# Performance work log

Hardware: AMD Instinct MI355X
Metric: run time of the kernel (lower is better)

## Reference

```python
import jax, jax.numpy as jnp
import numpy as np

N = 20000      # nodes
E = 80000      # edges (before self loops)
NG = 64        # graphs in batch
EMB = 780      # embedding_size (768 text + 12 time)
NEG_SLOPE = 0.2
BN_EPS = 1e-5


def setup_inputs() -> dict:
    key = jax.random.key(0)
    ks = jax.random.split(key, 20)
    def rn(k, shape, s=0.05):
        return jax.random.normal(k, shape, dtype=jnp.float32) * s
    z = lambda n: jnp.zeros((n,), dtype=jnp.float32)
    o = lambda n: jnp.ones((n,), dtype=jnp.float32)
    x = jax.random.normal(ks[0], (N, 772), dtype=jnp.float32)
    edge_index = jax.random.randint(ks[1], (2, E), 0, N)
    batch = jnp.sort(jax.random.randint(ks[2], (N,), 0, NG))
    return dict(
        x=x, edge_index=edge_index, batch=batch,
        time_W=rn(ks[3], (4, 12)), time_b=z(12),
        lin_W0=rn(ks[4], (EMB, 3 * EMB)), att_src0=rn(ks[5], (3, EMB)), att_dst0=rn(ks[6], (3, EMB)),
        bias0=z(3 * EMB), gamma0=o(3 * EMB), beta0=z(3 * EMB),
        lin_W1=rn(ks[7], (3 * EMB, 3 * EMB)), att_src1=rn(ks[8], (3, EMB)), att_dst1=rn(ks[9], (3, EMB)),
        bias1=z(3 * EMB), gamma1=o(3 * EMB), beta1=z(3 * EMB),
        lin_W2=rn(ks[10], (3 * EMB, EMB)), att_src2=rn(ks[11], (1, EMB)), att_dst2=rn(ks[12], (1, EMB)),
        bias2=z(EMB), gamma2=o(EMB), beta2=z(EMB),
        mlp_W1=rn(ks[13], (EMB, 128)), mlp_b1=z(128),
        mlp_W2=rn(ks[14], (128, 64)), mlp_b2=z(64),
    )


def _gat_layer(h, src, dst, W, a_src, a_dst, b, heads):
    # PyG GATConv (eval mode: dropout off), concat=True, self loops already in src/dst
    C = W.shape[1] // heads
    hp = (h @ W).reshape(N, heads, C)                       # [N,H,C]
    a_s = jnp.sum(hp * a_src[None], axis=-1)                # [N,H]
    a_d = jnp.sum(hp * a_dst[None], axis=-1)                # [N,H]
    e = jax.nn.leaky_relu(a_s[src] + a_d[dst], NEG_SLOPE)   # [E+N,H]
    m = jax.ops.segment_max(e, dst, num_segments=N)         # segment softmax over incoming edges
    m = jnp.where(jnp.isfinite(m), m, 0.0)
    p = jnp.exp(e - m[dst])
    denom = jax.ops.segment_sum(p, dst, num_segments=N)
    alpha = p / (denom[dst] + 1e-16)                        # [E+N,H]
    out = jax.ops.segment_sum(alpha[:, :, None] * hp[src], dst, num_segments=N)  # [N,H,C]
    return out.reshape(N, heads * C) + b


def _bn(h, gamma, beta):
    # BatchNorm in training-mode math (batch statistics, biased variance)
    mu = jnp.mean(h, axis=0)
    var = jnp.mean((h - mu) ** 2, axis=0)
    return (h - mu) * jax.lax.rsqrt(var + BN_EPS) * gamma + beta


def reference(x, edge_index, batch, time_W, time_b,
              lin_W0, att_src0, att_dst0, bias0, gamma0, beta0,
              lin_W1, att_src1, att_dst1, bias1, gamma1, beta1,
              lin_W2, att_src2, att_dst2, bias2, gamma2, beta2,
              mlp_W1, mlp_b1, mlp_W2, mlp_b2):
    te = x[:, 768:772] @ time_W + time_b
    h = jnp.concatenate([jax.lax.stop_gradient(x[:, :768]), te,
                         jax.lax.stop_gradient(x[:, 772:])], axis=-1)  # [N, 780]
    sl = jnp.arange(N)
    src = jnp.concatenate([edge_index[0], sl])   # add self loops
    dst = jnp.concatenate([edge_index[1], sl])
    layers = [
        (lin_W0, att_src0, att_dst0, bias0, gamma0, beta0, 3),
        (lin_W1, att_src1, att_dst1, bias1, gamma1, beta1, 3),
        (lin_W2, att_src2, att_dst2, bias2, gamma2, beta2, 1),
    ]
    for W, a_s, a_d, b, g, bt, heads in layers:
        h = jnp.tanh(_gat_layer(h, src, dst, W, a_s, a_d, b, heads))
        h = _bn(h, g, bt)
    cnt = jax.ops.segment_sum(jnp.ones((N,), dtype=h.dtype), batch, num_segments=NG)
    pooled = jax.ops.segment_sum(h, batch, num_segments=NG) / jnp.maximum(cnt, 1.0)[:, None]
    pooled = jax.nn.relu(pooled)
    out = jnp.tanh(pooled @ mlp_W1 + mlp_b1) @ mlp_W2 + mlp_b2
    return out  # [NG, 64]
```

## Files before the change

kernel.cpp:

```cpp
#include <hip/hip_runtime.h>
#include <math.h>

#define NN   20000
#define EE   80000
#define ELP  100000
#define NGR  64
#define EMB  780
#define W3   2340
#define EMBP 832
#define W3P  2368
#define NZ   (W3+8)

static inline int cdiv_i(long long a, long long b){ return (int)((a + b - 1) / b); }

typedef _Float16 f16;
typedef _Float16 f16x4 __attribute__((ext_vector_type(4)));
typedef _Float16 f16x8 __attribute__((ext_vector_type(8)));
typedef float    f32x4 __attribute__((ext_vector_type(4)));

__device__ __forceinline__ void async_ld16(const f16* g, f16* l){
    __builtin_amdgcn_global_load_lds(
        (const __attribute__((address_space(1))) unsigned int*)g,
        (__attribute__((address_space(3))) unsigned int*)l,
        16, 0, 0);
}

__global__ void k_zero_f32(float* p, int n){
    int i = blockIdx.x*256 + threadIdx.x; if (i < n) p[i] = 0.f;
}
__global__ void k_zero_i32(int* p, int n){
    int i = blockIdx.x*256 + threadIdx.x; if (i < n) p[i] = 0;
}
__global__ void k_copy_i32(const int* __restrict__ s, int* __restrict__ d, int n){
    int i = blockIdx.x*256 + threadIdx.x; if (i < n) d[i] = s[i];
}

__global__ void k_transpose(const float* __restrict__ W, f16* __restrict__ Wt,
                            const float* __restrict__ sc, int K, int N, int KP){
    __shared__ float T[32][33];
    int n0 = blockIdx.x*32, k0 = blockIdx.y*32;
    int tx = threadIdx.x, ty = threadIdx.y;
#pragma unroll
    for (int r = 0; r < 4; r++){
        int k = k0 + ty + r*8;
        float v = 0.f;
        if (k < K && n0 + tx < N){
            v = W[(size_t)k*N + n0 + tx];
            if (sc) v *= sc[k];
        }
        T[ty + r*8][tx] = v;
    }
    __syncthreads();
#pragma unroll
    for (int r = 0; r < 4; r++){
        int n = n0 + ty + r*8;
        int k = k0 + tx;
        if (n < N && k < KP) Wt[(size_t)n*KP + k] = (f16)T[tx][ty + r*8];
    }
}

__global__ void k_wvec(const float* __restrict__ W, const float* __restrict__ asrc,
                       const float* __restrict__ adst, const float* __restrict__ sc,
                       f16* __restrict__ Wt, int K, int N, int KP, int H){
    int k = blockIdx.x*4 + (threadIdx.x >> 6);
    int lane = threadIdx.x & 63;
    if (k >= K) return;
    const float* row = W + (size_t)k*N;
    float acc[6];
#pragma unroll
    for (int i = 0; i < 6; i++) acc[i] = 0.f;
    for (int c = lane; c < EMB; c += 64){
        for (int h = 0; h < H; h++){
            float wv = row[h*EMB + c];
            acc[h]     += wv * asrc[h*EMB + c];
            acc[H + h] += wv * adst[h*EMB + c];
        }
    }
    float s = sc ? sc[k] : 1.f;
    for (int i = 0; i < 2*H; i++){
        float v = acc[i];
#pragma unroll
        for (int off = 32; off; off >>= 1) v += __shfl_xor(v, off);
        if (lane == 0) Wt[(size_t)(N + i)*KP + k] = (f16)(v * s);
    }
}

__global__ void k_wfin(const float* __restrict__ asrc, const float* __restrict__ adst,
                       float* __restrict__ dvec, int N, int H){
    int wv = threadIdx.x >> 6, lane = threadIdx.x & 63;
    for (int i = wv; i < 2*H; i += 4){
        int h = (i < H) ? i : (i - H);
        const float* att = (i < H) ? (asrc + h*EMB) : (adst + h*EMB);
        float s = 0.f;
        for (int c = lane; c < EMB; c += 64) s += dvec[h*EMB + c] * att[c];
#pragma unroll
        for (int off = 32; off; off >>= 1) s += __shfl_xor(s, off);
        if (lane == 0) dvec[N + i] = s;
    }
}

#define DVEC_KSPLIT 32
__global__ void k_dvec(const float* __restrict__ W, const float* __restrict__ sh,
                       float* __restrict__ dvec, int K, int N){
    int n = blockIdx.x*256 + threadIdx.x;
    if (n >= N) return;
    int slice = blockIdx.y;
    int k0 = (int)(((long long)K * slice) / DVEC_KSPLIT);
    int k1 = (int)(((long long)K * (slice+1)) / DVEC_KSPLIT);
    float s = 0.f;
    for (int k = k0; k < k1; k++) s += sh[k] * W[(size_t)k*N + n];
    atomicAdd(&dvec[n], s);
}

__global__ void k_build_h(const float* __restrict__ x, const float* __restrict__ tW,
                          const float* __restrict__ tb, f16* __restrict__ h){
    int idx = blockIdx.x*256 + threadIdx.x;
    if (idx >= NN*EMBP) return;
    int n = idx / EMBP, c = idx - n*EMBP;
    const float* xr = x + (size_t)n*772;
    float v;
    if (c < 768) v = xr[c];
    else if (c < EMB){
        int j = c - 768;
        v = tb[j] + xr[768]*tW[j] + xr[769]*tW[12+j] + xr[770]*tW[24+j] + xr[771]*tW[36+j];
    } else v = 0.f;
    h[idx] = (f16)v;
}

__global__ void k_deg(const int* __restrict__ ei, int* __restrict__ deg){
    int k = blockIdx.x*256 + threadIdx.x; if (k >= ELP) return;
    int d = (k < EE) ? ei[EE + k] : (k - EE);
    atomicAdd(&deg[d], 1);
}

__global__ __launch_bounds__(1024) void k_scan(const int* __restrict__ deg, int* __restrict__ rp){
    __shared__ int part[1024];
    int tid = threadIdx.x;
    int i0 = tid*20;
    int n = (i0 < NN) ? min(20, NN - i0) : 0;
    int s = 0;
    for (int k = 0; k < n; k++) s += deg[i0+k];
    part[tid] = s; __syncthreads();
    for (int off = 1; off < 1024; off <<= 1){
        int t = (tid >= off) ? part[tid-off] : 0;
        __syncthreads();
        part[tid] += t;
        __syncthreads();
    }
    int run = part[tid] - s;
    for (int k = 0; k < n; k++){ rp[i0+k] = run; run += deg[i0+k]; }
    if (tid == 1023) rp[NN] = part[1023];
}

__global__ void k_fill(const int* __restrict__ ei, int* __restrict__ cursor, int* __restrict__ csrc){
    int k = blockIdx.x*256 + threadIdx.x; if (k >= ELP) return;
    int s, d;
    if (k < EE){ s = ei[k]; d = ei[EE + k]; } else { s = k - EE; d = s; }
    int pos = atomicAdd(&cursor[d], 1);
    csrc[pos] = s;
}

__global__ void k_grp(const int* __restrict__ batch, int* __restrict__ grp){
    int g = blockIdx.x*256 + threadIdx.x; if (g > NGR) return;
    int lo = 0, hi = NN;
    while (lo < hi){ int mid = (lo+hi)>>1; if (batch[mid] < g) lo = mid+1; else hi = mid; }
    grp[g] = lo;
}

__global__ __launch_bounds__(256) void k_gemm_mfma(const f16* __restrict__ A,
                                                   const f16* __restrict__ Bt,
                                                   const float* __restrict__ dvec,
                                                   f16* __restrict__ C,
                                                   float* __restrict__ a_sd,
                                                   int M, int N, int NB, int H,
                                                   int KP, int SN,
                                                   int Mtiles, int NT){
    int bid = blockIdx.x;
    int xcd = bid & 7;
    int j   = bid >> 3;
    int sl  = j / NT;
    int nt  = j - sl*NT;
    int mt  = sl*8 + xcd;
    if (mt >= Mtiles) return;
    int m0 = mt*128, n0 = nt*128;

    __shared__ f16 As[128*64];
    __shared__ f16 Bs[128*64];
    int tid = threadIdx.x;
    int w = tid >> 6, lane = tid & 63;

    int lrow = lane >> 2;
    int lko  = (lane & 3) * 8;

    int i2a = w*2, i2b = w*2 + 1;
    const f16* gA0 = A  + (size_t)min(m0 + i2a*16 + lrow, M-1)*KP + lko;
    const f16* gA1 = A  + (size_t)min(m0 + i2b*16 + lrow, M-1)*KP + lko;
    const f16* gB0 = Bt + (size_t)min(n0 + i2a*16 + lrow, NB-1)*KP + lko;
    const f16* gB1 = Bt + (size_t)min(n0 + i2b*16 + lrow, NB-1)*KP + lko;
    f16* lA0 = &As[i2a*512]; f16* lA1 = &As[i2b*512];
    f16* lB0 = &Bs[i2a*512]; f16* lB1 = &Bs[i2b*512];

    f32x4 acc[4][4];
#pragma unroll
    for (int i = 0; i < 4; i++)
#pragma unroll
        for (int j2 = 0; j2 < 4; j2++) acc[i][j2] = (f32x4)0.f;

    int wm = (w & 1) * 64, wn = (w >> 1) * 64;
    int lq = lane >> 4, lm = lane & 15;

    for (int kk = 0; kk < KP; kk += 64){
        __syncthreads();
        async_ld16(gA0 + kk, lA0);
        async_ld16(gA1 + kk, lA1);
        async_ld16(gB0 + kk, lB0);
        async_ld16(gB1 + kk, lB1);
        async_ld16(gA0 + kk + 32, lA0 + 4096);
        async_ld16(gA1 + kk + 32, lA1 + 4096);
        async_ld16(gB0 + kk + 32, lB0 + 4096);
        async_ld16(gB1 + kk + 32, lB1 + 4096);
        __syncthreads();

#pragma unroll
        for (int half = 0; half < 2; half++){
            const f16* Ap = As + half*4096;
            const f16* Bp = Bs + half*4096;
            f16x8 aF[4], bF[4];
#pragma unroll
            for (int mi = 0; mi < 4; mi++)
                aF[mi] = *(const f16x8*)&Ap[(wm + mi*16 + lm)*32 + lq*8];
#pragma unroll
            for (int ni = 0; ni < 4; ni++)
                bF[ni] = *(const f16x8*)&Bp[(wn + ni*16 + lm)*32 + lq*8];
#pragma unroll
            for (int mi = 0; mi < 4; mi++)
#pragma unroll
                for (int ni = 0; ni < 4; ni++)
                    acc[mi][ni] = __builtin_amdgcn_mfma_f32_16x16x32_f16(aF[mi], bF[ni], acc[mi][ni], 0, 0, 0);
        }
    }

#pragma unroll
    for (int mi = 0; mi < 4; mi++){
#pragma unroll
        for (int ni = 0; ni < 4; ni++){
            int col = n0 + wn + ni*16 + lm;
            int rbase = m0 + wm + mi*16 + lq*4;
            if (col < N){
                float dv = dvec[col];
#pragma unroll
                for (int r = 0; r < 4; r++){
                    int row = rbase + r;
                    if (row < M)
                        C[(size_t)row*SN + col] = (f16)(acc[mi][ni][r] + dv);
                }
            } else if (col < NB){
                int jc = col - N;
                int idx = (jc < H) ? jc : (3 + jc - H);
                float dv = dvec[col];
#pragma unroll
                for (int r = 0; r < 4; r++){
                    int row = rbase + r;
                    if (row < M)
                        a_sd[(size_t)row*6 + idx] = acc[mi][ni][r] + dv;
                }
            }
        }
    }
}

template<int H>
__global__ __launch_bounds__(256) void k_agg2(const f16* __restrict__ hp, const int* __restrict__ rp,
                                              const int* __restrict__ csrc, const float* __restrict__ a_sd,
                                              const float* __restrict__ bias,
                                              f16* __restrict__ y, int SP, int W){
    int n = blockIdx.x, tid = threadIdx.x, lane = tid & 63;
    int beg = rp[n], deg = rp[n+1] - beg;

    float adv[H];
#pragma unroll
    for (int h = 0; h < H; h++) adv[h] = a_sd[(size_t)n*6 + 3 + h];

    float mx[H];
#pragma unroll
    for (int h = 0; h < H; h++) mx[h] = -1e30f;
    for (int base = 0; base < deg; base += 64){
        int e = base + lane;
        if (e < deg){
            int s = csrc[beg + e];
#pragma unroll
            for (int h = 0; h < H; h++){
                float t = a_sd[(size_t)s*6 + h] + adv[h];
                t = t > 0.f ? t : 0.2f*t;
                mx[h] = fmaxf(mx[h], t);
            }
        }
    }
#pragma unroll
    for (int off = 32; off; off >>= 1)
#pragma unroll
        for (int h = 0; h < H; h++) mx[h] = fmaxf(mx[h], __shfl_xor(mx[h], off));

    float dn[H];
#pragma unroll
    for (int h = 0; h < H; h++) dn[h] = 0.f;
    for (int base = 0; base < deg; base += 64){
        int e = base + lane;
        if (e < deg){
            int s = csrc[beg + e];
#pragma unroll
            for (int h = 0; h < H; h++){
                float t = a_sd[(size_t)s*6 + h] + adv[h];
                t = t > 0.f ? t : 0.2f*t;
                dn[h] += expf(t - mx[h]);
            }
        }
    }
#pragma unroll
    for (int off = 32; off; off >>= 1)
#pragma unroll
        for (int h = 0; h < H; h++) dn[h] += __shfl_xor(dn[h], off);
    float inv[H];
#pragma unroll
    for (int h = 0; h < H; h++) inv[h] = 1.f / (dn[h] + 1e-16f);

    float acc[2][8];
#pragma unroll
    for (int g = 0; g < 2; g++)
#pragma unroll
        for (int j = 0; j < 8; j++) acc[g][j] = 0.f;
    int  cg[2];  cg[0] = tid*8; cg[1] = 2048 + tid*8;
    bool act[2]; act[0] = cg[0] < W; act[1] = cg[1] < W;
    int hlo[2], hhi[2], nsp[2];
#pragma unroll
    for (int g = 0; g < 2; g++){
        int c = cg[g];
        int hl = min(c / EMB, H-1);
        int hh = min((c+7) / EMB, H-1);
        hlo[g] = hl; hhi[g] = hh;
        nsp[g] = (hh > hl) ? (EMB*(hl+1) - c) : 8;
    }

    for (int base = 0; base < deg; base += 64){
        int cnt = min(64, deg - base);
        int sl = 0; float al[H];
        {
            int e = base + lane;
            if (e < deg){
                sl = csrc[beg + e];
#pragma unroll
                for (int h = 0; h < H; h++){
                    float t = a_sd[(size_t)sl*6 + h] + adv[h];
                    t = t > 0.f ? t : 0.2f*t;
                    al[h] = expf(t - mx[h]) * inv[h];
                }
            } else {
#pragma unroll
                for (int h = 0; h < H; h++) al[h] = 0.f;
            }
        }
#pragma unroll 2
        for (int e = 0; e < cnt; e++){
            int s = __shfl(sl, e);
            float a0 = __shfl(al[0], e);
            float a1 = (H==3) ? __shfl(al[1], e) : a0;
            float a2 = (H==3) ? __shfl(al[2], e) : a0;
            const f16* row = hp + (size_t)s*SP;
#pragma unroll
            for (int g = 0; g < 2; g++){
                if (act[g]){
                    f16x8 v = *(const f16x8*)(row + cg[g]);
                    float lo = (hlo[g]==0) ? a0 : (hlo[g]==1 ? a1 : a2);
                    float hi = (hhi[g]==0) ? a0 : (hhi[g]==1 ? a1 : a2);
#pragma unroll
                    for (int j = 0; j < 8; j++){
                        float alj = (j < nsp[g]) ? lo : hi;
                        acc[g][j] += alj * (float)v[j];
                    }
                }
            }
        }
    }

#pragma unroll
    for (int g = 0; g < 2; g++){
        int c = cg[g];
        if (c < SP){
            f16x8 o;
#pragma unroll
            for (int j = 0; j < 8; j++){
                float vv = (c + j < W) ? tanhf(acc[g][j] + bias[c+j]) : 0.f;
                o[j] = (f16)vv;
            }
            *(f16x8*)(y + (size_t)n*SP + c) = o;
        }
    }
}

__global__ void k_bnstat(const f16* __restrict__ y, float* __restrict__ ps,
                         float* __restrict__ pq, int W, int SP){
    int c0 = (blockIdx.x*256 + threadIdx.x)*4;
    if (c0 >= W) return;
    int slice = blockIdx.y;
    float s[4] = {0,0,0,0}, q[4] = {0,0,0,0};
    for (int r = slice; r < NN; r += 128){
        f16x4 u = *(const f16x4*)(y + (size_t)r*SP + c0);
#pragma unroll
        for (int j = 0; j < 4; j++){ float v = (float)u[j]; s[j] += v; q[j] += v*v; }
    }
#pragma unroll
    for (int j = 0; j < 4; j++){
        ps[(size_t)slice*W3 + c0+j] = s[j];
        pq[(size_t)slice*W3 + c0+j] = q[j];
    }
}

__global__ void k_bnfin(const float* __restrict__ ps, const float* __restrict__ pq,
                        const float* __restrict__ gamma, const float* __restrict__ beta,
                        float* __restrict__ sc, float* __restrict__ sh,
                        float* __restrict__ dvec, int W, int zn){
    int c = blockIdx.x*256 + threadIdx.x;
    if (c < W){
        float m = 0.f, q = 0.f;
        for (int s = 0; s < 128; s++){ m += ps[(size_t)s*W3 + c]; q += pq[(size_t)s*W3 + c]; }
        m *= (1.f/NN);
        float v = q * (1.f/NN) - m*m;
        float is = 1.f / sqrtf(v + 1e-5f);
        float g = gamma[c];
        sc[c] = is * g;
        sh[c] = beta[c] - m * is * g;
    }
    if (c < zn) dvec[c] = 0.f;
}

__global__ void k_pool(const f16* __restrict__ h, const int* __restrict__ grp,
                       float* __restrict__ pooled){
    int g = blockIdx.x;
    int c = threadIdx.x*4;
    if (c >= EMB) return;
    int r0 = grp[g], r1 = grp[g+1];
    float s0=0.f, s1=0.f, s2=0.f, s3=0.f;
    for (int r = r0; r < r1; r++){
        f16x4 u = *(const f16x4*)(h + (size_t)r*EMBP + c);
        s0 += (float)u[0]; s1 += (float)u[1]; s2 += (float)u[2]; s3 += (float)u[3];
    }
    pooled[g*EMB + c] = s0; pooled[g*EMB + c+1] = s1;
    pooled[g*EMB + c+2] = s2; pooled[g*EMB + c+3] = s3;
}

__global__ __launch_bounds__(256) void k_mlp(const float* __restrict__ pooled, const int* __restrict__ grp,
                                             const float* __restrict__ sc, const float* __restrict__ sh,
                                             const float* __restrict__ W1, const float* __restrict__ b1,
                                             const float* __restrict__ W2, const float* __restrict__ b2,
                                             float* __restrict__ out){
    __shared__ float p[EMB];
    __shared__ float hid[128];
    int g = blockIdx.x, tid = threadIdx.x;
    int cnt = grp[g+1] - grp[g];
    float ic = 1.f / fmaxf((float)cnt, 1.f);
    for (int c = tid; c < EMB; c += 256){
        float v = pooled[g*EMB + c] * ic * sc[c] + sh[c];
        p[c] = v > 0.f ? v : 0.f;
    }
    __syncthreads();
    if (tid < 128){
        float s = b1[tid];
        for (int k = 0; k < EMB; k++) s += p[k] * W1[k*128 + tid];
        hid[tid] = tanhf(s);
    }
    __syncthreads();
    if (tid < 64){
        float s = b2[tid];
        for (int k = 0; k < 128; k++) s += hid[k] * W2[k*64 + tid];
        out[g*64 + tid] = s;
    }
}

extern "C" void kernel_launch(void* const* d_in, const int* in_sizes, int n_in,
                              void* d_out, int out_size, void* d_ws, size_t ws_size,
                              hipStream_t stream) {
    (void)in_sizes; (void)n_in; (void)out_size;
    const float* x    = (const float*)d_in[0];
    const int*   ei   = (const int*)  d_in[1];
    const int*   batch= (const int*)  d_in[2];
    const float* tW   = (const float*)d_in[3];
    const float* tb   = (const float*)d_in[4];
    const float* W0   = (const float*)d_in[5];
    const float* as0  = (const float*)d_in[6];
    const float* ad0  = (const float*)d_in[7];
    const float* b0   = (const float*)d_in[8];
    const float* g0   = (const float*)d_in[9];
    const float* be0  = (const float*)d_in[10];
    const float* W1   = (const float*)d_in[11];
    const float* as1  = (const float*)d_in[12];
    const float* ad1  = (const float*)d_in[13];
    const float* b1   = (const float*)d_in[14];
    const float* g1   = (const float*)d_in[15];
    const float* be1  = (const float*)d_in[16];
    const float* W2   = (const float*)d_in[17];
    const float* as2  = (const float*)d_in[18];
    const float* ad2  = (const float*)d_in[19];
    const float* b2   = (const float*)d_in[20];
    const float* g2   = (const float*)d_in[21];
    const float* be2  = (const float*)d_in[22];
    const float* mW1  = (const float*)d_in[23];
    const float* mb1  = (const float*)d_in[24];
    const float* mW2  = (const float*)d_in[25];
    const float* mb2  = (const float*)d_in[26];
    float* outp = (float*)d_out;

    size_t off = 0;
    auto carve = [&](size_t bytes) -> void* {
        void* p = (char*)d_ws + off;
        off = (off + bytes + 255) & ~(size_t)255;
        return p;
    };
    f16* big1 = (f16*)carve((size_t)NN*W3P*2);
    f16* big2 = (f16*)carve((size_t)NN*W3P*2);
    f16* Wt   = (f16*)carve((size_t)NZ*W3P*2);
    float* a_sd  = (float*)carve((size_t)NN*6*4);
    float* psum  = (float*)carve((size_t)128*W3*4);
    float* psq   = (float*)carve((size_t)128*W3*4);
    float* sc    = (float*)carve((size_t)W3*4);
    float* sh    = (float*)carve((size_t)W3*4);
    float* dvec  = (float*)carve((size_t)NZ*4);
    float* pooled= (float*)carve((size_t)NGR*EMB*4);
    int*   grp   = (int*)carve((size_t)(NGR+1)*4);
    int*   deg   = (int*)carve((size_t)NN*4);
    int*   rp    = (int*)carve((size_t)(NN+1)*4);
    int*   csrc  = (int*)carve((size_t)ELP*4);

    if (ws_size < off) return;

    k_zero_i32<<<cdiv_i(NN,256),256,0,stream>>>(deg, NN);
    k_deg<<<cdiv_i(ELP,256),256,0,stream>>>(ei, deg);
    k_scan<<<1,1024,0,stream>>>(deg, rp);
    k_copy_i32<<<cdiv_i(NN,256),256,0,stream>>>(rp, deg, NN);
    k_fill<<<cdiv_i(ELP,256),256,0,stream>>>(ei, deg, csrc);
    k_grp<<<1,256,0,stream>>>(batch, grp);

    k_build_h<<<cdiv_i((long long)NN*EMBP,256),256,0,stream>>>(x, tW, tb, big1);
    k_zero_f32<<<cdiv_i(NZ,256),256,0,stream>>>(dvec, NZ);

    struct Layer { const float* W; const float* as; const float* ad; const float* b;
                   const float* g; const float* be; int H; int K; int KP; };
    Layer layers[3] = {
        {W0, as0, ad0, b0, g0, be0, 3, EMB, EMBP},
        {W1, as1, ad1, b1, g1, be1, 3, W3,  W3P },
        {W2, as2, ad2, b2, g2, be2, 1, W3,  W3P },
    };

    for (int L = 0; L < 3; L++){
        Layer& ly = layers[L];
        int Wout  = ly.H * EMB;
        int NB    = Wout + 2*ly.H;
        int SPout = (Wout == W3) ? W3P : EMBP;
        const float* scale = (L == 0) ? nullptr : sc;

        dim3 tg(cdiv_i(Wout,32), cdiv_i(ly.KP,32));
        k_transpose<<<tg, dim3(32,8), 0, stream>>>(ly.W, Wt, scale, ly.K, Wout, ly.KP);
        k_wvec<<<cdiv_i(ly.K,4),256,0,stream>>>(ly.W, ly.as, ly.ad, scale, Wt, ly.K, Wout, ly.KP, ly.H);
        if (L > 0){
            dim3 dg(cdiv_i(Wout,256), DVEC_KSPLIT);
            k_dvec<<<dg,256,0,stream>>>(ly.W, sh, dvec, ly.K, Wout);
        }
        k_wfin<<<1,256,0,stream>>>(ly.as, ly.ad, dvec, Wout, ly.H);

        int Mtiles = cdiv_i(NN,128), NT = cdiv_i(NB,128);
        int nb = ((Mtiles+7)/8)*8*NT;
        k_gemm_mfma<<<nb, 256, 0, stream>>>(big1, Wt, dvec, big2, a_sd,
                                            NN, Wout, NB, ly.H, ly.KP, SPout, Mtiles, NT);

        if (ly.H == 3)
            k_agg2<3><<<NN,256,0,stream>>>(big2, rp, csrc, a_sd, ly.b, big1, SPout, Wout);
        else
            k_agg2<1><<<NN,256,0,stream>>>(big2, rp, csrc, a_sd, ly.b, big1, SPout, Wout);

        dim3 gs(cdiv_i(Wout/4,256), 128);
        k_bnstat<<<gs,256,0,stream>>>(big1, psum, psq, Wout, SPout);
        int zn = (L < 2) ? NZ : 0;
        k_bnfin<<<cdiv_i(Wout,256),256,0,stream>>>(psum, psq, ly.g, ly.be, sc, sh, dvec, Wout, zn);
    }

    k_pool<<<NGR,256,0,stream>>>(big1, grp, pooled);
    k_mlp<<<NGR,256,0,stream>>>(pooled, grp, sc, sh, mW1, mb1, mW2, mb2, outp);
}
```

Baseline: 1.651 ms.

## Fuse weight-prep kernels, stage GEMM epilogue through LDS, vectorize build and scan copy

Folds the BN-shift dvec reduction into the transpose kernel and the attention-vector finalisation into k_wvec, and lets the scan write the cursor array directly, removing several small launches. The GEMM epilogue now stages the f16 output tile in LDS and writes it with 16-byte stores instead of scattered 2-byte stores. k_build_h writes 4 halves per thread, bnstat reads contiguous row ranges, and the aggregation loop is unrolled further. There is a race risk: k_wvec block 0 reads dvec that k_transpose fills with atomics, which relies on stream ordering, and the wfin part can run before the other wvec blocks finish, though those blocks do not write dvec.

```diff
diff --git a/kernel.cpp b/kernel.cpp
--- a/kernel.cpp
+++ b/kernel.cpp
@@ -31,24 +31,31 @@
 __global__ void k_zero_i32(int* p, int n){
     int i = blockIdx.x*256 + threadIdx.x; if (i < n) p[i] = 0;
 }
-__global__ void k_copy_i32(const int* __restrict__ s, int* __restrict__ d, int n){
-    int i = blockIdx.x*256 + threadIdx.x; if (i < n) d[i] = s[i];
-}
 
 __global__ void k_transpose(const float* __restrict__ W, f16* __restrict__ Wt,
-                            const float* __restrict__ sc, int K, int N, int KP){
+                            const float* __restrict__ sc, const float* __restrict__ sh,
+                            float* __restrict__ dvec, int K, int N, int KP){
     __shared__ float T[32][33];
+    __shared__ float D[8][33];
     int n0 = blockIdx.x*32, k0 = blockIdx.y*32;
     int tx = threadIdx.x, ty = threadIdx.y;
+    float raw[4];
 #pragma unroll
     for (int r = 0; r < 4; r++){
         int k = k0 + ty + r*8;
-        float v = 0.f;
-        if (k < K && n0 + tx < N){
-            v = W[(size_t)k*N + n0 + tx];
-            if (sc) v *= sc[k];
-        }
-        T[ty + r*8][tx] = v;
+        float w = 0.f;
+        if (k < K && n0 + tx < N) w = W[(size_t)k*N + n0 + tx];
+        raw[r] = w;
+        T[ty + r*8][tx] = sc ? w * ((k < K) ? sc[k] : 0.f) : w;
+    }
+    if (sh){
+        float p = 0.f;
+#pragma unroll
+        for (int r = 0; r < 4; r++){
+            int k = k0 + ty + r*8;
+            if (k < K) p += sh[k] * raw[r];
+        }
+        D[ty][tx] = p;
     }
     __syncthreads();
 #pragma unroll
@@ -57,74 +64,74 @@
         int k = k0 + tx;
         if (n < N && k < KP) Wt[(size_t)n*KP + k] = (f16)T[tx][ty + r*8];
     }
+    if (sh && ty == 0 && n0 + tx < N){
+        float s = 0.f;
+#pragma unroll
+        for (int j = 0; j < 8; j++) s += D[j][tx];
+        atomicAdd(&dvec[n0 + tx], s);
+    }
 }
 
 __global__ void k_wvec(const float* __restrict__ W, const float* __restrict__ asrc,
                        const float* __restrict__ adst, const float* __restrict__ sc,
-                       f16* __restrict__ Wt, int K, int N, int KP, int H){
+                       f16* __restrict__ Wt, float* __restrict__ dvec,
+                       int K, int N, int KP, int H){
     int k = blockIdx.x*4 + (threadIdx.x >> 6);
     int lane = threadIdx.x & 63;
-    if (k >= K) return;
-    const float* row = W + (size_t)k*N;
-    float acc[6];
-#pragma unroll
-    for (int i = 0; i < 6; i++) acc[i] = 0.f;
-    for (int c = lane; c < EMB; c += 64){
-        for (int h = 0; h < H; h++){
-            float wv = row[h*EMB + c];
-            acc[h]     += wv * asrc[h*EMB + c];
-            acc[H + h] += wv * adst[h*EMB + c];
-        }
-    }
-    float s = sc ? sc[k] : 1.f;
-    for (int i = 0; i < 2*H; i++){
-        float v = acc[i];
-#pragma unroll
-        for (int off = 32; off; off >>= 1) v += __shfl_xor(v, off);
-        if (lane == 0) Wt[(size_t)(N + i)*KP + k] = (f16)(v * s);
-    }
-}
-
-__global__ void k_wfin(const float* __restrict__ asrc, const float* __restrict__ adst,
-                       float* __restrict__ dvec, int N, int H){
-    int wv = threadIdx.x >> 6, lane = threadIdx.x & 63;
-    for (int i = wv; i < 2*H; i += 4){
-        int h = (i < H) ? i : (i - H);
-        const float* att = (i < H) ? (asrc + h*EMB) : (adst + h*EMB);
-        float s = 0.f;
-        for (int c = lane; c < EMB; c += 64) s += dvec[h*EMB + c] * att[c];
-#pragma unroll
-        for (int off = 32; off; off >>= 1) s += __shfl_xor(s, off);
-        if (lane == 0) dvec[N + i] = s;
-    }
-}
-
-#define DVEC_KSPLIT 32
-__global__ void k_dvec(const float* __restrict__ W, const float* __restrict__ sh,
-                       float* __restrict__ dvec, int K, int N){
-    int n = blockIdx.x*256 + threadIdx.x;
-    if (n >= N) return;
-    int slice = blockIdx.y;
-    int k0 = (int)(((long long)K * slice) / DVEC_KSPLIT);
-    int k1 = (int)(((long long)K * (slice+1)) / DVEC_KSPLIT);
-    float s = 0.f;
-    for (int k = k0; k < k1; k++) s += sh[k] * W[(size_t)k*N + n];
-    atomicAdd(&dvec[n], s);
+    if (k < K){
+        const float* row = W + (size_t)k*N;
+        float acc[6];
+#pragma unroll
+        for (int i = 0; i < 6; i++) acc[i] = 0.f;
+        for (int c = lane; c < EMB; c += 64){
+            for (int h = 0; h < H; h++){
+                float wv = row[h*EMB + c];
+                acc[h]     += wv * asrc[h*EMB + c];
+                acc[H + h] += wv * adst[h*EMB + c];
+            }
+        }
+        float s = sc ? sc[k] : 1.f;
+        for (int i = 0; i < 2*H; i++){
+            float v = acc[i];
+#pragma unroll
+            for (int off = 32; off; off >>= 1) v += __shfl_xor(v, off);
+            if (lane == 0) Wt[(size_t)(N + i)*KP + k] = (f16)(v * s);
+        }
+    }
+    if (blockIdx.x == 0){
+        int wv = threadIdx.x >> 6;
+        for (int i = wv; i < 2*H; i += 4){
+            int h = (i < H) ? i : (i - H);
+            const float* att = (i < H) ? (asrc + h*EMB) : (adst + h*EMB);
+            float s = 0.f;
+            for (int c = lane; c < EMB; c += 64) s += dvec[h*EMB + c] * att[c];
+#pragma unroll
+            for (int off = 32; off; off >>= 1) s += __shfl_xor(s, off);
+            if (lane == 0) dvec[N + i] = s;
+        }
+    }
 }
 
 __global__ void k_build_h(const float* __restrict__ x, const float* __restrict__ tW,
                           const float* __restrict__ tb, f16* __restrict__ h){
     int idx = blockIdx.x*256 + threadIdx.x;
-    if (idx >= NN*EMBP) return;
-    int n = idx / EMBP, c = idx - n*EMBP;
+    int total = NN*(EMBP/4);
+    if (idx >= total) return;
+    int n = idx / (EMBP/4);
+    int c0 = (idx - n*(EMBP/4))*4;
     const float* xr = x + (size_t)n*772;
-    float v;
-    if (c < 768) v = xr[c];
-    else if (c < EMB){
-        int j = c - 768;
-        v = tb[j] + xr[768]*tW[j] + xr[769]*tW[12+j] + xr[770]*tW[24+j] + xr[771]*tW[36+j];
-    } else v = 0.f;
-    h[idx] = (f16)v;
+    f16x4 o;
+#pragma unroll
+    for (int j = 0; j < 4; j++){
+        int c = c0 + j; float v;
+        if (c < 768) v = xr[c];
+        else if (c < EMB){
+            int t = c - 768;
+            v = tb[t] + xr[768]*tW[t] + xr[769]*tW[12+t] + xr[770]*tW[24+t] + xr[771]*tW[36+t];
+        } else v = 0.f;
+        o[j] = (f16)v;
+    }
+    *(f16x4*)(h + (size_t)n*EMBP + c0) = o;
 }
 
 __global__ void k_deg(const int* __restrict__ ei, int* __restrict__ deg){
@@ -133,7 +140,7 @@
     atomicAdd(&deg[d], 1);
 }
 
-__global__ __launch_bounds__(1024) void k_scan(const int* __restrict__ deg, int* __restrict__ rp){
+__global__ __launch_bounds__(1024) void k_scan(int* __restrict__ deg, int* __restrict__ rp){
     __shared__ int part[1024];
     int tid = threadIdx.x;
     int i0 = tid*20;
@@ -148,7 +155,12 @@
         __syncthreads();
     }
     int run = part[tid] - s;
-    for (int k = 0; k < n; k++){ rp[i0+k] = run; run += deg[i0+k]; }
+    for (int k = 0; k < n; k++){
+        int d = deg[i0+k];
+        rp[i0+k] = run;
+        deg[i0+k] = run;
+        run += d;
+    }
     if (tid == 1023) rp[NN] = part[1023];
 }
 
@@ -184,8 +196,9 @@
     if (mt >= Mtiles) return;
     int m0 = mt*128, n0 = nt*128;
 
-    __shared__ f16 As[128*64];
-    __shared__ f16 Bs[128*64];
+    __shared__ f16 smem[128*136];
+    f16* As = smem;
+    f16* Bs = smem + 8192;
     int tid = threadIdx.x;
     int w = tid >> 6, lane = tid & 63;
 
@@ -245,24 +258,50 @@
 #pragma unroll
         for (int ni = 0; ni < 4; ni++){
             int col = n0 + wn + ni*16 + lm;
-            int rbase = m0 + wm + mi*16 + lq*4;
-            if (col < N){
-                float dv = dvec[col];
-#pragma unroll
-                for (int r = 0; r < 4; r++){
-                    int row = rbase + r;
-                    if (row < M)
-                        C[(size_t)row*SN + col] = (f16)(acc[mi][ni][r] + dv);
-                }
-            } else if (col < NB){
+            if (col >= N && col < NB){
                 int jc = col - N;
                 int idx = (jc < H) ? jc : (3 + jc - H);
                 float dv = dvec[col];
+                int rbase = m0 + wm + mi*16 + lq*4;
 #pragma unroll
                 for (int r = 0; r < 4; r++){
                     int row = rbase + r;
-                    if (row < M)
-                        a_sd[(size_t)row*6 + idx] = acc[mi][ni][r] + dv;
+                    if (row < M) a_sd[(size_t)row*6 + idx] = acc[mi][ni][r] + dv;
+                }
+            }
+        }
+    }
+
+    if (n0 < N){
+        __syncthreads();
+#pragma unroll
+        for (int mi = 0; mi < 4; mi++){
+#pragma unroll
+            for (int ni = 0; ni < 4; ni++){
+                int col = wn + ni*16 + lm;
+                int gcol = n0 + col;
+                float dv = (gcol < N) ? dvec[gcol] : 0.f;
+#pragma unroll
+                for (int r = 0; r < 4; r++){
+                    int row = wm + mi*16 + lq*4 + r;
+                    smem[row*136 + col] = (f16)(acc[mi][ni][r] + dv);
+                }
+            }
+        }
+        __syncthreads();
+        int ncols = min(128, N - n0);
+#pragma unroll
+        for (int it = 0; it < 8; it++){
+            int ch = tid + it*256;
+            int row = ch >> 4, cc = (ch & 15)*8;
+            int grow = m0 + row;
+            if (grow < M && cc < ncols){
+                if (cc + 8 <= ncols){
+                    f16x8 v = *(f16x8*)&smem[row*136 + cc];
+                    *(f16x8*)(C + (size_t)grow*SN + n0 + cc) = v;
+                } else {
+                    for (int jj = cc; jj < ncols; jj++)
+                        C[(size_t)grow*SN + n0 + jj] = smem[row*136 + jj];
                 }
             }
         }
@@ -359,7 +398,7 @@
                 for (int h = 0; h < H; h++) al[h] = 0.f;
             }
         }
-#pragma unroll 2
+#pragma unroll 4
         for (int e = 0; e < cnt; e++){
             int s = __shfl(sl, e);
             float a0 = __shfl(al[0], e);
@@ -402,8 +441,10 @@
     int c0 = (blockIdx.x*256 + threadIdx.x)*4;
     if (c0 >= W) return;
     int slice = blockIdx.y;
+    int r0 = (int)(((long long)NN*slice)/128);
+    int r1 = (int)(((long long)NN*(slice+1))/128);
     float s[4] = {0,0,0,0}, q[4] = {0,0,0,0};
-    for (int r = slice; r < NN; r += 128){
+    for (int r = r0; r < r1; r++){
         f16x4 u = *(const f16x4*)(y + (size_t)r*SP + c0);
 #pragma unroll
         for (int j = 0; j < 4; j++){ float v = (float)u[j]; s[j] += v; q[j] += v*v; }
@@ -535,11 +576,10 @@
     k_zero_i32<<<cdiv_i(NN,256),256,0,stream>>>(deg, NN);
     k_deg<<<cdiv_i(ELP,256),256,0,stream>>>(ei, deg);
     k_scan<<<1,1024,0,stream>>>(deg, rp);
-    k_copy_i32<<<cdiv_i(NN,256),256,0,stream>>>(rp, deg, NN);
     k_fill<<<cdiv_i(ELP,256),256,0,stream>>>(ei, deg, csrc);
     k_grp<<<1,256,0,stream>>>(batch, grp);
 
-    k_build_h<<<cdiv_i((long long)NN*EMBP,256),256,0,stream>>>(x, tW, tb, big1);
+    k_build_h<<<cdiv_i((long long)NN*(EMBP/4),256),256,0,stream>>>(x, tW, tb, big1);
     k_zero_f32<<<cdiv_i(NZ,256),256,0,stream>>>(dvec, NZ);
 
     struct Layer { const float* W; const float* as; const float* ad; const float* b;
@@ -556,15 +596,11 @@
         int NB    = Wout + 2*ly.H;
         int SPout = (Wout == W3) ? W3P : EMBP;
         const float* scale = (L == 0) ? nullptr : sc;
+        const float* shift = (L == 0) ? nullptr : sh;
 
         dim3 tg(cdiv_i(Wout,32), cdiv_i(ly.KP,32));
-        k_transpose<<<tg, dim3(32,8), 0, stream>>>(ly.W, Wt, scale, ly.K, Wout, ly.KP);
-        k_wvec<<<cdiv_i(ly.K,4),256,0,stream>>>(ly.W, ly.as, ly.ad, scale, Wt, ly.K, Wout, ly.KP, ly.H);
-        if (L > 0){
-            dim3 dg(cdiv_i(Wout,256), DVEC_KSPLIT);
-            k_dvec<<<dg,256,0,stream>>>(ly.W, sh, dvec, ly.K, Wout);
-        }
-        k_wfin<<<1,256,0,stream>>>(ly.as, ly.ad, dvec, Wout, ly.H);
+        k_transpose<<<tg, dim3(32,8), 0, stream>>>(ly.W, Wt, scale, shift, dvec, ly.K, Wout, ly.KP);
+        k_wvec<<<cdiv_i(ly.K,4),256,0,stream>>>(ly.W, ly.as, ly.ad, scale, Wt, dvec, ly.K, Wout, ly.KP, ly.H);
 
         int Mtiles = cdiv_i(NN,128), NT = cdiv_i(NB,128);
         int nb = ((Mtiles+7)/8)*8*NT;
```

Measured after the change: 1.490 ms. 1.11x faster.
